# Kernel optimization log

Hardware: AMD Instinct MI355X
Metric: run time of the kernel (lower is better)

## Reference

```python
import jax, jax.numpy as jnp
import numpy as np

N_RES = 4096
BATCH = 1024
N_IN = 128
N_OUT = 64
TEACHER_SHIFT = 0.0
TEACHER_SCALE = 1.0
PREV_STATE_WEIGHT = 0.1
SPECTRAL_RADIUS = 0.95


def setup_inputs() -> dict:
    key = jax.random.key(0)
    ks = jax.random.split(key, 9)
    # Reservoir weights, scaled to fixed spectral radius (as in build()).
    W_res = jax.random.uniform(ks[0], (N_RES, N_RES), minval=-0.5, maxval=0.5, dtype=jnp.float32)
    e = jnp.linalg.eigvalsh(W_res)  # tf.linalg.eigh also treats matrix as symmetric
    W_res = W_res * (SPECTRAL_RADIUS / jnp.max(jnp.abs(e)))
    W_in = jax.random.uniform(ks[1], (N_RES, N_IN), minval=-1.0, maxval=1.0, dtype=jnp.float32)
    W_out = jax.random.uniform(ks[2], (N_RES, N_OUT), minval=-1.0, maxval=1.0, dtype=jnp.float32)
    B_in = 0.1 * jax.random.normal(ks[3], (N_RES, 1), dtype=jnp.float32)
    return {
        "passed": jax.random.normal(ks[4], (BATCH, N_IN), dtype=jnp.float32),
        "lastOutput": jax.random.normal(ks[5], (N_OUT, BATCH), dtype=jnp.float32),
        "lastPredOutput": jax.random.normal(ks[6], (N_OUT, BATCH), dtype=jnp.float32),
        "x": jax.random.normal(ks[7], (BATCH, N_RES), dtype=jnp.float32),
        "prob": 50.0 * jnp.ones((1,), dtype=jnp.float32),
        "rand_num": jax.random.uniform(ks[8], (1,), minval=1.0, maxval=100.0, dtype=jnp.float32),
        "W_in": W_in,
        "W_res": W_res,
        "W_out": W_out,
        "B_in": B_in,
    }


def reference(passed, lastOutput, lastPredOutput, x, prob, rand_num, W_in, W_res, W_out, B_in):
    # Teacher forcing selection (tf.case on random draw vs prob), applied after scale/shift.
    last_true = lastOutput * TEACHER_SCALE + TEACHER_SHIFT      # [n_out, B]
    last_pred = lastPredOutput * TEACHER_SCALE + TEACHER_SHIFT  # [n_out, B]
    toUse = jnp.where(rand_num[0] < prob[0], last_true, last_pred)  # [n_out, B]

    # Batched version of the per-sample loop:
    #   tanh(W_in@u_i + W_res@x_i + W_out@toUse[:,i] + B_in)
    pre = (passed @ W_in.T            # [B, N] input drive
           + x @ W_res.T              # [B, N] recurrent drive
           + toUse.T @ W_out.T        # [B, N] output feedback
           + B_in[:, 0][None, :])     # [1, N] bias
    new_state = PREV_STATE_WEIGHT * x + (1.0 - PREV_STATE_WEIGHT) * jnp.tanh(pre)
    return new_state  # [B, N]; original returns this split into B [1,N] tensors
```

## Files before the change

kernel.cpp:

```cpp
#include <hip/hip_runtime.h>
#include <hip/hip_bf16.h>
#include <math.h>

#define NRES   4096
#define NBATCH 1024
#define NIN    128
#define NOUT   64
#define KT     4672
#define KQ     (KT / 4)
#define TILES  73
#define MN     ((size_t)NBATCH * NRES)

typedef __bf16 bf16x8 __attribute__((ext_vector_type(8)));
typedef __bf16 bf16x4 __attribute__((ext_vector_type(4)));
typedef float  f32x4  __attribute__((ext_vector_type(4)));

__device__ __forceinline__ float lo_part(float f) {
    return f - (float)(__bf16)f;
}

__device__ __forceinline__ void gload_lds16(const __bf16* g, __bf16* l) {
    __builtin_amdgcn_global_load_lds(
        (const __attribute__((address_space(1))) unsigned int*)g,
        (__attribute__((address_space(3))) unsigned int*)l, 16, 0, 0);
}

#define BU ((unsigned)NRES * KQ)
#define AU ((unsigned)NBATCH * KQ)

__global__ __launch_bounds__(256) void pack_all(
    const float* __restrict__ x, const float* __restrict__ passed,
    const float* __restrict__ lastOut, const float* __restrict__ lastPred,
    const float* __restrict__ prob, const float* __restrict__ rand_num,
    const float* __restrict__ W_res, const float* __restrict__ W_in,
    const float* __restrict__ W_out,
    __bf16* __restrict__ Abuf, __bf16* __restrict__ Bbuf)
{
    unsigned id = blockIdx.x * 256u + threadIdx.x;
    f32x4 v;
    __bf16* dst;
    if (id < BU) {
        unsigned n = id / KQ;
        unsigned k = (id - n * KQ) * 4u;
        if (k < 4096u) {
            v = *(const f32x4*)(W_res + (size_t)n * NRES + k);
        } else if (k < 4224u) {
            v = *(const f32x4*)(W_in + n * NIN + (k - 4096u));
        } else if (k < 4352u) {
            f32x4 f = *(const f32x4*)(W_in + n * NIN + (k - 4224u));
#pragma unroll
            for (int e = 0; e < 4; ++e) v[e] = lo_part(f[e]);
        } else if (k < 4480u) {
            v = *(const f32x4*)(W_in + n * NIN + (k - 4352u));
        } else if (k < 4544u) {
            v = *(const f32x4*)(W_out + n * NOUT + (k - 4480u));
        } else if (k < 4608u) {
            f32x4 f = *(const f32x4*)(W_out + n * NOUT + (k - 4544u));
#pragma unroll
            for (int e = 0; e < 4; ++e) v[e] = lo_part(f[e]);
        } else {
            v = *(const f32x4*)(W_out + n * NOUT + (k - 4608u));
        }
        dst = Bbuf + (size_t)id * 4u;
    } else {
        unsigned aid = id - BU;
        if (aid >= AU) return;
        unsigned b = aid / KQ;
        unsigned k = (aid - b * KQ) * 4u;
        if (k < 4096u) {
            v = *(const f32x4*)(x + (size_t)b * NRES + k);
        } else if (k < 4224u) {
            v = *(const f32x4*)(passed + b * NIN + (k - 4096u));
        } else if (k < 4352u) {
            v = *(const f32x4*)(passed + b * NIN + (k - 4224u));
        } else if (k < 4480u) {
            f32x4 f = *(const f32x4*)(passed + b * NIN + (k - 4352u));
#pragma unroll
            for (int e = 0; e < 4; ++e) v[e] = lo_part(f[e]);
        } else {
            const float* src = (rand_num[0] < prob[0]) ? lastOut : lastPred;
#pragma unroll
            for (int e = 0; e < 4; ++e) {
                unsigned kk = k + e;
                unsigned j; bool want_lo;
                if (kk < 4544u)      { j = kk - 4480u; want_lo = false; }
                else if (kk < 4608u) { j = kk - 4544u; want_lo = false; }
                else                 { j = kk - 4608u; want_lo = true;  }
                float f = src[j * NBATCH + b];
                v[e] = want_lo ? lo_part(f) : f;
            }
        }
        dst = Abuf + (size_t)aid * 4u;
    }
    bf16x4 o;
#pragma unroll
    for (int e = 0; e < 4; ++e) o[e] = (__bf16)v[e];
    *(bf16x4*)dst = o;
}

__global__ __launch_bounds__(512, 1) void gemm_kernel(
    const __bf16* __restrict__ Abuf, const __bf16* __restrict__ Bbuf,
    __bf16* __restrict__ part, int split)
{
    __shared__ __align__(16) __bf16 SH[2][32768];

    const int t  = threadIdx.x;
    const int l  = t & 63;
    const int w  = t >> 6;
    const int wm = w >> 2;
    const int wn = w & 3;

    const int nwg  = gridDim.x * gridDim.y * gridDim.z;
    const int cpx  = nwg >> 3;
    const int flat = blockIdx.x + gridDim.x * (blockIdx.y + gridDim.y * blockIdx.z);
    const int o    = (flat & 7) * cpx + (flat >> 3);
    const int bn   = o % gridDim.x;
    const int bm   = (o / gridDim.x) % gridDim.y;
    const int bz   = o / (gridDim.x * gridDim.y);

    const int qs = TILES / split, rs = TILES % split;
    const int t0 = bz * qs + (bz < rs ? bz : rs);
    const int nt = qs + (bz < rs ? 1 : 0);

    f32x4 acc[8][4] = {};

    unsigned goff[4][2];
    int lE[4][2];
#pragma unroll
    for (int c = 0; c < 4; ++c) {
#pragma unroll
        for (int j = 0; j < 2; ++j) {
            int ui = j * 512 + t;
            int lr = ui >> 3;
            int cb = (ui & 7) << 4;
            int rc;
            if (c == 0)      rc = (lr & 63) + ((lr >> 6) << 7);
            else if (c == 1) rc = 64 + (lr & 63) + ((lr >> 6) << 7);
            else if (c == 2) rc = (lr & 31) + ((lr >> 5) << 6);
            else             rc = 32 + (lr & 31) + ((lr >> 5) << 6);
            int cs = cb ^ ((rc & 7) << 4);
            if (c < 2) {
                goff[c][j] = (unsigned)((bm * 256 + rc) * KT) + (cs >> 1);
                lE[c][j]   = rc * 64 + (cb >> 1);
            } else {
                goff[c][j] = (unsigned)((bn * 256 + rc) * KT) + (cs >> 1);
                lE[c][j]   = 16384 + rc * 64 + (cb >> 1);
            }
        }
    }

#define STAGEC(c, nxt, k0n)                                              \
    do {                                                                 \
        gload_lds16(((c) < 2 ? Abuf : Bbuf) + goff[c][0] + (k0n),        \
                    &SH[nxt][lE[c][0]]);                                 \
        gload_lds16(((c) < 2 ? Abuf : Bbuf) + goff[c][1] + (k0n),        \
                    &SH[nxt][lE[c][1]]);                                 \
    } while (0)

    int eA[8], eB[4];
#pragma unroll
    for (int m = 0; m < 8; ++m) {
        int row = wm * 128 + m * 16 + (l & 15);
        eA[m] = row * 64 + (((((l >> 4) << 4)) ^ ((row & 7) << 4)) >> 1);
    }
#pragma unroll
    for (int n = 0; n < 4; ++n) {
        int col = wn * 64 + n * 16 + (l & 15);
        eB[n] = 16384 + col * 64 + (((((l >> 4) << 4)) ^ ((col & 7) << 4)) >> 1);
    }

    bf16x8 af[4][2], bfr[4][2];

#define BAR() do { asm volatile("" ::: "memory");                        \
                   __builtin_amdgcn_s_barrier();                         \
                   asm volatile("" ::: "memory"); } while (0)
#define VM(n) asm volatile("s_waitcnt vmcnt(" #n ")" ::: "memory")

#define LDA(qd, buf)                                                     \
    do {                                                                 \
        _Pragma("unroll")                                                \
        for (int m2 = 0; m2 < 4; ++m2) {                                 \
            af[m2][0] = *(const bf16x8*)&SH[buf][eA[(qd)*4 + m2]];       \
            af[m2][1] = *(const bf16x8*)&SH[buf][eA[(qd)*4 + m2] ^ 32];  \
        }                                                                \
    } while (0)

#define LDB(h, buf)                                                      \
    do {                                                                 \
        _Pragma("unroll")                                                \
        for (int n3 = 0; n3 < 2; ++n3) {                                 \
            bfr[(h)*2+n3][0] = *(const bf16x8*)&SH[buf][eB[(h)*2 + n3]]; \
            bfr[(h)*2+n3][1] = *(const bf16x8*)&SH[buf][eB[(h)*2+n3] ^ 32]; \
        }                                                                \
    } while (0)

#define MFMA16(qm, qn)                                                   \
    do {                                                                 \
        __builtin_amdgcn_s_setprio(1);                                   \
        _Pragma("unroll")                                                \
        for (int kk2 = 0; kk2 < 2; ++kk2)                                \
            _Pragma("unroll")                                            \
            for (int m2 = 0; m2 < 4; ++m2)                               \
                _Pragma("unroll")                                        \
                for (int n2 = 0; n2 < 2; ++n2)                           \
                    acc[(qm)*4+m2][(qn)*2+n2] =                          \
                        __builtin_amdgcn_mfma_f32_16x16x32_bf16(         \
                            af[m2][kk2], bfr[(qn)*2+n2][kk2],            \
                            acc[(qm)*4+m2][(qn)*2+n2], 0, 0, 0);         \
        __builtin_amdgcn_s_setprio(0);                                   \
    } while (0)

    {
        const int k00 = t0 * 64;
        STAGEC(0, 0, k00); STAGEC(2, 0, k00); STAGEC(3, 0, k00); STAGEC(1, 0, k00);
        VM(4);
        BAR();
    }

    for (int tt = 0; tt < nt - 1; ++tt) {
        const int cur = tt & 1;
        const int nxt = cur ^ 1;
        const int k0n = (t0 + tt + 1) * 64;
        LDA(0, cur); LDB(0, cur);
        STAGEC(0, nxt, k0n);
        VM(4);
        BAR();
        MFMA16(0, 0);
        LDB(1, cur);
        STAGEC(2, nxt, k0n);
        VM(4);
        BAR();
        MFMA16(0, 1);
        LDA(1, cur);
        STAGEC(3, nxt, k0n);
        MFMA16(1, 0);
        STAGEC(1, nxt, k0n);
        VM(4);
        BAR();
        MFMA16(1, 1);
    }
    {
        const int cur = (nt - 1) & 1;
        LDA(0, cur); LDB(0, cur);
        VM(2);
        BAR();
        MFMA16(0, 0);
        LDB(1, cur);
        VM(0);
        BAR();
        MFMA16(0, 1);
        LDA(1, cur);
        MFMA16(1, 0);
        MFMA16(1, 1);
    }

    __bf16* pz = part + (size_t)bz * MN;
    const int r0 = bm * 256 + wm * 128 + ((l >> 4) << 2);
    const int c0 = bn * 256 + wn * 64 + (l & 15);
#pragma unroll
    for (int m = 0; m < 8; ++m) {
#pragma unroll
        for (int i = 0; i < 4; ++i) {
            __bf16* prow = pz + (size_t)(r0 + m * 16 + i) * NRES;
#pragma unroll
            for (int n = 0; n < 4; ++n)
                prow[c0 + n * 16] = (__bf16)acc[m][n][i];
        }
    }
#undef STAGEC
#undef BAR
#undef VM
#undef LDA
#undef LDB
#undef MFMA16
}

__global__ __launch_bounds__(256) void epilogue_kernel(
    const __bf16* __restrict__ part, int split, const float* __restrict__ xin,
    const float* __restrict__ Bin, float* __restrict__ out)
{
    size_t id = (size_t)blockIdx.x * 256u + threadIdx.x;
    size_t e  = id * 8;
    int c = (int)(e & (NRES - 1));
    float s[8] = {};
    for (int z = 0; z < split; ++z) {
        bf16x8 p = *(const bf16x8*)(part + (size_t)z * MN + e);
#pragma unroll
        for (int j = 0; j < 8; ++j) s[j] += (float)p[j];
    }
    f32x4 xv0 = *(const f32x4*)(xin + e);
    f32x4 xv1 = *(const f32x4*)(xin + e + 4);
    f32x4 bv0 = *(const f32x4*)(Bin + c);
    f32x4 bv1 = *(const f32x4*)(Bin + c + 4);
    f32x4 o0, o1;
#pragma unroll
    for (int j = 0; j < 4; ++j) {
        o0[j] = 0.1f * xv0[j] + 0.9f * tanhf(s[j]     + bv0[j]);
        o1[j] = 0.1f * xv1[j] + 0.9f * tanhf(s[j + 4] + bv1[j]);
    }
    *(f32x4*)(out + e)     = o0;
    *(f32x4*)(out + e + 4) = o1;
}

extern "C" void kernel_launch(void* const* d_in, const int* in_sizes, int n_in,
                              void* d_out, int out_size, void* d_ws, size_t ws_size,
                              hipStream_t stream) {
    (void)in_sizes; (void)n_in; (void)out_size;
    const float* passed     = (const float*)d_in[0];
    const float* lastOutput = (const float*)d_in[1];
    const float* lastPred   = (const float*)d_in[2];
    const float* x          = (const float*)d_in[3];
    const float* prob       = (const float*)d_in[4];
    const float* rand_num   = (const float*)d_in[5];
    const float* W_in       = (const float*)d_in[6];
    const float* W_res      = (const float*)d_in[7];
    const float* W_out      = (const float*)d_in[8];
    const float* B_in       = (const float*)d_in[9];
    float* out = (float*)d_out;

    const size_t AB = (size_t)(NBATCH + NRES) * KT * 2;
    __bf16* Abuf = (__bf16*)d_ws;
    __bf16* Bbuf = (__bf16*)((char*)d_ws + (size_t)NBATCH * KT * 2);
    __bf16* part = (__bf16*)((char*)d_ws + AB);

    int split = 1;
    if (ws_size >= AB + 4 * MN * sizeof(__bf16))      split = 4;
    else if (ws_size >= AB + 2 * MN * sizeof(__bf16)) split = 2;

    pack_all<<<(BU + AU) / 256, 256, 0, stream>>>(
        x, passed, lastOutput, lastPred, prob, rand_num,
        W_res, W_in, W_out, Abuf, Bbuf);

    dim3 grid(NRES / 256, NBATCH / 256, split);
    gemm_kernel<<<grid, 512, 0, stream>>>(Abuf, Bbuf, part, split);

    epilogue_kernel<<<2048, 256, 0, stream>>>(part, split, x, B_in, out);
}
```

Measured before the change: 74.65 us.

## Store GEMM partials in fragment-native layout with vectorized writes, remap epilogue

The GEMM's split-K partial stores now use a tile-blocked, MFMA-fragment-native layout. Each lane writes contiguous 4-element bf16 vectors instead of scattered 2-byte stores strided by rows. The epilogue decodes this layout: it reads the partials contiguously and scatters the final fp32 outputs and x reads with per-element strided accesses. This trades uncoalesced partial writes in the GEMM for less coalesced output and x accesses in the epilogue.

```diff
diff --git a/kernel.cpp b/kernel.cpp
--- a/kernel.cpp
+++ b/kernel.cpp
@@ -254,18 +254,24 @@
         MFMA16(1, 1);
     }
 
-    __bf16* pz = part + (size_t)bz * MN;
-    const int r0 = bm * 256 + wm * 128 + ((l >> 4) << 2);
-    const int c0 = bn * 256 + wn * 64 + (l & 15);
-#pragma unroll
-    for (int m = 0; m < 8; ++m) {
-#pragma unroll
-        for (int i = 0; i < 4; ++i) {
-            __bf16* prow = pz + (size_t)(r0 + m * 16 + i) * NRES;
-#pragma unroll
-            for (int n = 0; n < 4; ++n)
-                prow[c0 + n * 16] = (__bf16)acc[m][n][i];
+    {
+        const int blk = (int)(o % (gridDim.x * gridDim.y));
+        __bf16* pz = part + (size_t)bz * MN
+                   + (size_t)(bm * (int)gridDim.x + bn) * 65536
+                   + (size_t)(w * 8192 + l * 4);
+#pragma unroll
+        for (int m = 0; m < 8; ++m) {
+#pragma unroll
+            for (int n = 0; n < 4; ++n) {
+                bf16x4 ov;
+                ov[0] = (__bf16)acc[m][n][0];
+                ov[1] = (__bf16)acc[m][n][1];
+                ov[2] = (__bf16)acc[m][n][2];
+                ov[3] = (__bf16)acc[m][n][3];
+                *(bf16x4*)(pz + m * 1024 + n * 256) = ov;
+            }
         }
+        (void)blk;
     }
 #undef STAGEC
 #undef BAR
@@ -279,27 +285,28 @@
     const __bf16* __restrict__ part, int split, const float* __restrict__ xin,
     const float* __restrict__ Bin, float* __restrict__ out)
 {
-    size_t id = (size_t)blockIdx.x * 256u + threadIdx.x;
-    size_t e  = id * 8;
-    int c = (int)(e & (NRES - 1));
-    float s[8] = {};
+    unsigned q = blockIdx.x * 256u + threadIdx.x;
+    unsigned blk = q >> 14;
+    unsigned w   = (q >> 11) & 7u;
+    unsigned m   = (q >> 8) & 7u;
+    unsigned n   = (q >> 6) & 3u;
+    unsigned l   = q & 63u;
+    unsigned r0  = (blk >> 4) * 256u + (w >> 2) * 128u + m * 16u + (l >> 4) * 4u;
+    unsigned c   = (blk & 15u) * 256u + (w & 3u) * 64u + n * 16u + (l & 15u);
+
+    size_t e = (size_t)q * 4;
+    float s[4] = {};
     for (int z = 0; z < split; ++z) {
-        bf16x8 p = *(const bf16x8*)(part + (size_t)z * MN + e);
-#pragma unroll
-        for (int j = 0; j < 8; ++j) s[j] += (float)p[j];
-    }
-    f32x4 xv0 = *(const f32x4*)(xin + e);
-    f32x4 xv1 = *(const f32x4*)(xin + e + 4);
-    f32x4 bv0 = *(const f32x4*)(Bin + c);
-    f32x4 bv1 = *(const f32x4*)(Bin + c + 4);
-    f32x4 o0, o1;
-#pragma unroll
-    for (int j = 0; j < 4; ++j) {
-        o0[j] = 0.1f * xv0[j] + 0.9f * tanhf(s[j]     + bv0[j]);
-        o1[j] = 0.1f * xv1[j] + 0.9f * tanhf(s[j + 4] + bv1[j]);
-    }
-    *(f32x4*)(out + e)     = o0;
-    *(f32x4*)(out + e + 4) = o1;
+        bf16x4 p = *(const bf16x4*)(part + (size_t)z * MN + e);
+#pragma unroll
+        for (int i = 0; i < 4; ++i) s[i] += (float)p[i];
+    }
+    float bc = Bin[c];
+#pragma unroll
+    for (int i = 0; i < 4; ++i) {
+        size_t oi = (size_t)(r0 + i) * NRES + c;
+        out[oi] = 0.1f * xin[oi] + 0.9f * tanhf(s[i] + bc);
+    }
 }
 
 extern "C" void kernel_launch(void* const* d_in, const int* in_sizes, int n_in,
@@ -334,5 +341,6 @@
     dim3 grid(NRES / 256, NBATCH / 256, split);
     gemm_kernel<<<grid, 512, 0, stream>>>(Abuf, Bbuf, part, split);
 
-    epilogue_kernel<<<2048, 256, 0, stream>>>(part, split, x, B_in, out);
-}
+    epilogue_kernel<<<(unsigned)(MN / 4 / 256), 256, 0, stream>>>(
+        part, split, x, B_in, out);
+}
```

Result: faster. 72.44 us (-3.0%).
